# Performance work log

Measured on AMD Instinct MI355X. Metric: run time of the kernel, lower is better.

## Reference

```python
import jax, jax.numpy as jnp
import numpy as np

B, N, A, H, HID = 2048, 8, 16, 32, 64   # batch, n_agents, dim_action, dim_utility_hidden, dim_hidden
DQ = (H + A) * N                         # dim_q_input


def setup_inputs() -> dict:
    key = jax.random.key(0)
    ks = jax.random.split(key, 6)
    def w(k, shape, fan_in):
        return jax.random.normal(k, shape, jnp.float32) / np.sqrt(fan_in).astype(np.float32)
    return {
        "hidden_states_n": jax.random.normal(ks[0], (B, N, H), jnp.float32),
        # one-hot actions, as QTRAN substitutes torch.eye(dim_action) rows
        "actions_n": jax.nn.one_hot(jax.random.randint(ks[1], (B, N), 0, A), A, dtype=jnp.float32),
        "q_w1": w(ks[2], (DQ, HID), DQ), "q_b1": jnp.zeros((HID,), jnp.float32),
        "q_w2": w(ks[3], (HID, HID), HID), "q_b2": jnp.zeros((HID,), jnp.float32),
        "q_w3": w(ks[4], (HID, 1), HID), "q_b3": jnp.zeros((1,), jnp.float32),
    }


def reference(hidden_states_n, actions_n, q_w1, q_b1, q_w2, q_b2, q_w3, q_b3):
    """Vectorized QTRAN_alt.counterfactual_values_hat.

    Original: for each agent g and action a, replace agent g's action with one-hot(a)
    and run the joint Q_jt MLP. Here all n_agents*dim_action substitutions are
    built by broadcasting and run as one batched MLP.
    Output: [B, n_agents, dim_action].
    """
    Bn, Nn, Hh = hidden_states_n.shape
    Aa = actions_n.shape[-1]
    eye_a = jnp.eye(Aa, dtype=actions_n.dtype)          # [a, dA]
    agent_eq = jnp.eye(Nn, dtype=bool)                  # [g, j]: j == g
    # cf_actions[b, g, a, j, :] = eye_a[a] if j == g else actions_n[b, j, :]
    cf_actions = jnp.where(
        agent_eq[None, :, None, :, None],               # [1,G,1,J,1]
        eye_a[None, None, :, None, :],                  # [1,1,A,1,dA]
        actions_n[:, None, None, :, :],                 # [B,1,1,J,dA]
    )                                                   # [B,G,A,J,dA]
    hid = jnp.broadcast_to(hidden_states_n[:, None, None, :, :], (Bn, Nn, Aa, Nn, Hh))
    # per-agent (hidden, action) concat then flatten agents, matching
    # torch.cat([h, a], -1).view([-1, dim_q_input])
    inp = jnp.concatenate([hid, cf_actions], axis=-1).reshape(Bn, Nn, Aa, Nn * (Hh + Aa))
    h1 = jax.nn.relu(inp @ q_w1 + q_b1)
    h2 = jax.nn.relu(h1 @ q_w2 + q_b2)
    q = h2 @ q_w3 + q_b3                                # [B, G, A, 1]
    return q[..., 0]
```

## Files before the change

### kernel.cpp

```cpp
#include <hip/hip_runtime.h>
#include <hip/hip_bf16.h>

typedef __attribute__((ext_vector_type(4))) float f32x4;
typedef __attribute__((ext_vector_type(8))) short bf16x8;

struct Smem {
    float inp[384];
    float part[4][64];
    float base[64];
    float subsum[64];
    float sub[8][64];
    int   sel[8];
};

template<bool ISF32>
__device__ __forceinline__ float ldin(const void* p, int i) {
    if constexpr (ISF32) return ((const float*)p)[i];
    else return __bfloat162float(((const __hip_bfloat16*)p)[i]);
}

template<bool ISF32>
__device__ __forceinline__ f32x4 ldq(const void* p, int i) {
    if constexpr (ISF32) return *(const f32x4*)((const float*)p + i);
    else {
        const __hip_bfloat16* q = (const __hip_bfloat16*)p + i;
        return (f32x4){__bfloat162float(q[0]), __bfloat162float(q[1]),
                       __bfloat162float(q[2]), __bfloat162float(q[3])};
    }
}

__device__ __forceinline__ short bf16bits(float v) {
    __hip_bfloat16 h = __float2bfloat16(v);
    return *(const short*)&h;
}
__device__ __forceinline__ float bf16val(short s) {
    return __bfloat162float(*(const __hip_bfloat16*)&s);
}

__device__ __forceinline__ bool word_looks_bf16(unsigned int w) {
    const unsigned int lo = w & 0xFFFFu;
    const unsigned int ex = (lo >> 7) & 0xFFu;
    return (ex >= 100u && ex <= 140u) || (lo & 0x7FFFu) == 0u;
}

__device__ __forceinline__ bool vote_isf32_scalar(const void* hidden) {
    const unsigned int* hw = (const unsigned int*)hidden;
    int cnt = 0;
    #pragma unroll
    for (int i = 0; i < 32; ++i) cnt += word_looks_bf16(hw[i]) ? 1 : 0;
    return cnt < 16;
}

template<bool ISF32>
__device__ void w2prep_body(const void* w2, short* wsfrag, int idx0) {
    #pragma unroll
    for (int i = 0; i < 2; ++i) {
        const int idx = idx0 + i * 2048;
        const int j = idx & 7;
        const int lane = (idx >> 3) & 63;
        const int nt = (idx >> 9) & 3;
        const int ks = idx >> 11;
        const int src = (ks * 32 + (lane >> 4) * 8 + j) * 64 + nt * 16 + (lane & 15);
        const float v = ldin<ISF32>(w2, src);
        const short hb = bf16bits(v);
        wsfrag[idx] = hb;
        wsfrag[4096 + idx] = bf16bits(v - bf16val(hb));
    }
}

__global__ __launch_bounds__(256) void w2prep_kernel(
    const void* __restrict__ hidden, const void* __restrict__ w2,
    short* __restrict__ wsfrag) {
    const int idx0 = blockIdx.x * 256 + threadIdx.x;
    if (vote_isf32_scalar(hidden)) w2prep_body<true>(w2, wsfrag, idx0);
    else                           w2prep_body<false>(w2, wsfrag, idx0);
}

template<bool ISF32>
__device__ void qtran_body(Smem& sm,
    const void* __restrict__ hidden, const void* __restrict__ actions,
    const void* __restrict__ w1, const void* __restrict__ b1,
    const void* __restrict__ w2, const void* __restrict__ b2,
    const void* __restrict__ w3, const void* __restrict__ b3,
    void* __restrict__ out, const short* __restrict__ wsfrag, int b, int t)
{
    const int lane = t & 63;
    const int wv = t >> 6;
    const int q = lane >> 4;
    const int n = lane & 15;
    const int fq = lane & 15;
    const int rofs = lane >> 4;

    f32x4 wr[2][2][2];
    #pragma unroll
    for (int mt = 0; mt < 2; ++mt) {
        const int row = ((wv * 2 + mt) * 48 + 32 + n) * 64;
        #pragma unroll
        for (int ks = 0; ks < 2; ++ks) {
            wr[mt][ks][0] = ldq<ISF32>(w1, row + ks * 32 + q * 8);
            wr[mt][ks][1] = ldq<ISF32>(w1, row + ks * 32 + q * 8 + 4);
        }
    }
    float b2f[4], w3f[4];
    #pragma unroll
    for (int nt = 0; nt < 4; ++nt) {
        b2f[nt] = ldin<ISF32>(b2, nt * 16 + n);
        w3f[nt] = ldin<ISF32>(w3, nt * 16 + n);
    }
    const float b3f = ldin<ISF32>(b3, 0);

    if (t < 64) {
        const int j = t >> 3, k4 = (t & 7) * 4;
        *(f32x4*)&sm.inp[j * 48 + k4] = ldq<ISF32>(hidden, (b * 8 + j) * 32 + k4);
    } else if (t < 96) {
        const int i = t - 64;
        const int j = i >> 2, c4 = (i & 3) * 4;
        *(f32x4*)&sm.inp[j * 48 + 32 + c4] = ldq<ISF32>(actions, (b * 8 + j) * 16 + c4);
    }
    __syncthreads();

    if (t < 128) {
        const int g = t >> 4, a = t & 15;
        if (sm.inp[g * 48 + 32 + a] > 0.5f) sm.sel[g] = a;
    }
    {
        f32x4 a4 = (f32x4){0.f, 0.f, 0.f, 0.f};
        #pragma unroll 8
        for (int p = 0; p < 16; ++p) {
            const int hr = wv * 64 + p * 4 + rofs;
            const int r = (hr >> 5) * 48 + (hr & 31);
            const float xv = sm.inp[r];
            const f32x4 wq = ldq<ISF32>(w1, r * 64 + fq * 4);
            #pragma unroll
            for (int c = 0; c < 4; ++c) a4[c] = fmaf(xv, wq[c], a4[c]);
        }
        #pragma unroll
        for (int c = 0; c < 4; ++c) {
            a4[c] += __shfl_xor(a4[c], 16);
            a4[c] += __shfl_xor(a4[c], 32);
        }
        if (rofs == 0) *(f32x4*)&sm.part[wv][fq * 4] = a4;
    }
    __syncthreads();

    if (t < 128) {
        const int g = t >> 4, f4 = (t & 15) * 4;
        *(f32x4*)&sm.sub[g][f4] =
            ldq<ISF32>(w1, (g * 48 + 32 + sm.sel[g]) * 64 + f4);
    } else if (t < 192) {
        const int f = t - 128;
        sm.base[f] = ldin<ISF32>(b1, f) + sm.part[0][f] + sm.part[1][f]
                   + sm.part[2][f] + sm.part[3][f];
    } else {
        const int f = t - 192;
        float s = 0.f;
        #pragma unroll
        for (int g = 0; g < 8; ++g)
            s += ldin<ISF32>(w1, (g * 48 + 32 + sm.sel[g]) * 64 + f);
        sm.subsum[f] = s;
    }
    __syncthreads();

    f32x4 bsA[2][2];
    #pragma unroll
    for (int ks = 0; ks < 2; ++ks)
      #pragma unroll
      for (int h = 0; h < 2; ++h) {
        const int f0 = ks * 32 + q * 8 + h * 4;
        const f32x4 bb = *(const f32x4*)&sm.base[f0];
        const f32x4 ss = *(const f32x4*)&sm.subsum[f0];
        bsA[ks][h] = (f32x4){bb[0] + ss[0], bb[1] + ss[1], bb[2] + ss[2], bb[3] + ss[3]};
      }
    bf16x8 ahi[2][2];
    #pragma unroll
    for (int mt = 0; mt < 2; ++mt) {
        const int g = wv * 2 + mt;
        #pragma unroll
        for (int ks = 0; ks < 2; ++ks) {
            #pragma unroll
            for (int h = 0; h < 2; ++h) {
                const int f0 = ks * 32 + q * 8 + h * 4;
                const f32x4 sg = *(const f32x4*)&sm.sub[g][f0];
                const f32x4 w4 = wr[mt][ks][h];
                #pragma unroll
                for (int c = 0; c < 4; ++c) {
                    const float v = fmaxf(bsA[ks][h][c] - sg[c] + w4[c], 0.f);
                    ahi[ks][mt][h * 4 + c] = bf16bits(v);
                }
            }
        }
    }

    f32x4 acc[2][4];
    #pragma unroll
    for (int mt = 0; mt < 2; ++mt)
      #pragma unroll
      for (int nt = 0; nt < 4; ++nt)
        acc[mt][nt] = (f32x4){0.f, 0.f, 0.f, 0.f};

    #pragma unroll
    for (int ks = 0; ks < 2; ++ks) {
        #pragma unroll
        for (int nt = 0; nt < 4; ++nt) {
            bf16x8 bhi, blo;
            if (wsfrag) {
                const int fb = ((ks * 4 + nt) * 64 + lane) * 8;
                bhi = *(const bf16x8*)&wsfrag[fb];
                blo = *(const bf16x8*)&wsfrag[4096 + fb];
            } else {
                #pragma unroll
                for (int j = 0; j < 8; ++j) {
                    const float v = ldin<ISF32>(w2, (ks * 32 + q * 8 + j) * 64 + nt * 16 + n);
                    const short hb = bf16bits(v);
                    bhi[j] = hb;
                    blo[j] = bf16bits(v - bf16val(hb));
                }
            }
            #pragma unroll
            for (int mt = 0; mt < 2; ++mt) {
                acc[mt][nt] = __builtin_amdgcn_mfma_f32_16x16x32_bf16(
                    ahi[ks][mt], bhi, acc[mt][nt], 0, 0, 0);
                acc[mt][nt] = __builtin_amdgcn_mfma_f32_16x16x32_bf16(
                    ahi[ks][mt], blo, acc[mt][nt], 0, 0, 0);
            }
        }
    }

    #pragma unroll
    for (int mt = 0; mt < 2; ++mt) {
      #pragma unroll
      for (int r = 0; r < 4; ++r) {
        float p = 0.f;
        #pragma unroll
        for (int nt = 0; nt < 4; ++nt) {
            const float h2 = fmaxf(acc[mt][nt][r] + b2f[nt], 0.f);
            p = fmaf(h2, w3f[nt], p);
        }
        p += __shfl_xor(p, 1);
        p += __shfl_xor(p, 2);
        p += __shfl_xor(p, 4);
        p += __shfl_xor(p, 8);
        if (n == mt * 4 + r) {
            const int item = wv * 32 + mt * 16 + q * 4 + r;
            if constexpr (ISF32) ((float*)out)[b * 128 + item] = p + b3f;
            else ((__hip_bfloat16*)out)[b * 128 + item] = __float2bfloat16(p + b3f);
        }
      }
    }
}

__global__ __launch_bounds__(256, 4) void qtran_cf_kernel(
    const void* __restrict__ hidden, const void* __restrict__ actions,
    const void* __restrict__ w1, const void* __restrict__ b1,
    const void* __restrict__ w2, const void* __restrict__ b2,
    const void* __restrict__ w3, const void* __restrict__ b3,
    void* __restrict__ out, const short* __restrict__ wsfrag)
{
    __shared__ Smem sm;
    const unsigned int* hw = (const unsigned int*)hidden;
    const bool pass = word_looks_bf16(hw[threadIdx.x & 31]);
    const unsigned long long m = __ballot(pass);
    const bool isf32 = (__popcll(m) < 32);

    const int b = blockIdx.x;
    const int t = threadIdx.x;
    if (isf32)
        qtran_body<true>(sm, hidden, actions, w1, b1, w2, b2, w3, b3, out, wsfrag, b, t);
    else
        qtran_body<false>(sm, hidden, actions, w1, b1, w2, b2, w3, b3, out, wsfrag, b, t);
}

extern "C" void kernel_launch(void* const* d_in, const int* in_sizes, int n_in,
                              void* d_out, int out_size, void* d_ws, size_t ws_size,
                              hipStream_t stream) {
    short* wsfrag = (ws_size >= 16384) ? (short*)d_ws : nullptr;
    if (wsfrag)
        w2prep_kernel<<<8, 256, 0, stream>>>(d_in[0], d_in[4], wsfrag);
    qtran_cf_kernel<<<2048, 256, 0, stream>>>(
        d_in[0], d_in[1], d_in[2], d_in[3], d_in[4], d_in[5], d_in[6], d_in[7],
        d_out, wsfrag);
}
```

Baseline: 90.26 us.

## Process four batch rows per block with shared W1 action slice in LDS

Each block now handles four batch items instead of one. The W2 MFMA fragments stay in registers, and the W1 action rows (128x64) are staged once into padded LDS, so their load cost is spread across the four items. Each wave then loops over the eight agents for its own batch item. The grid shrinks to 512 blocks and the occupancy hint drops to 2, which reduces parallelism and raises LDS use per block in exchange for less repeated global weight traffic.

```diff
diff --git a/kernel.cpp b/kernel.cpp
--- a/kernel.cpp
+++ b/kernel.cpp
@@ -4,13 +4,16 @@
 typedef __attribute__((ext_vector_type(4))) float f32x4;
 typedef __attribute__((ext_vector_type(8))) short bf16x8;
 
+#define NB 4
+#define W1A_S 68
+
 struct Smem {
-    float inp[384];
-    float part[4][64];
-    float base[64];
-    float subsum[64];
-    float sub[8][64];
-    int   sel[8];
+    float inp[NB][384];
+    float part[4][NB][64];
+    float baseAll[NB][64];
+    float sub[NB][8][64];
+    __align__(16) float w1act[128 * W1A_S];
+    int sel[NB][8];
 };
 
 template<bool ISF32>
@@ -82,174 +85,186 @@
     const void* __restrict__ w1, const void* __restrict__ b1,
     const void* __restrict__ w2, const void* __restrict__ b2,
     const void* __restrict__ w3, const void* __restrict__ b3,
-    void* __restrict__ out, const short* __restrict__ wsfrag, int b, int t)
+    void* __restrict__ out, const short* __restrict__ wsfrag, int blk, int t)
 {
     const int lane = t & 63;
     const int wv = t >> 6;
     const int q = lane >> 4;
     const int n = lane & 15;
-    const int fq = lane & 15;
-    const int rofs = lane >> 4;
-
-    f32x4 wr[2][2][2];
-    #pragma unroll
-    for (int mt = 0; mt < 2; ++mt) {
-        const int row = ((wv * 2 + mt) * 48 + 32 + n) * 64;
-        #pragma unroll
-        for (int ks = 0; ks < 2; ++ks) {
-            wr[mt][ks][0] = ldq<ISF32>(w1, row + ks * 32 + q * 8);
-            wr[mt][ks][1] = ldq<ISF32>(w1, row + ks * 32 + q * 8 + 4);
-        }
-    }
-    float b2f[4], w3f[4];
-    #pragma unroll
-    for (int nt = 0; nt < 4; ++nt) {
-        b2f[nt] = ldin<ISF32>(b2, nt * 16 + n);
-        w3f[nt] = ldin<ISF32>(w3, nt * 16 + n);
-    }
-    const float b3f = ldin<ISF32>(b3, 0);
-
-    if (t < 64) {
-        const int j = t >> 3, k4 = (t & 7) * 4;
-        *(f32x4*)&sm.inp[j * 48 + k4] = ldq<ISF32>(hidden, (b * 8 + j) * 32 + k4);
-    } else if (t < 96) {
-        const int i = t - 64;
-        const int j = i >> 2, c4 = (i & 3) * 4;
-        *(f32x4*)&sm.inp[j * 48 + 32 + c4] = ldq<ISF32>(actions, (b * 8 + j) * 16 + c4);
-    }
-    __syncthreads();
-
-    if (t < 128) {
-        const int g = t >> 4, a = t & 15;
-        if (sm.inp[g * 48 + 32 + a] > 0.5f) sm.sel[g] = a;
-    }
-    {
-        f32x4 a4 = (f32x4){0.f, 0.f, 0.f, 0.f};
+    const int fq = n;
+    const int rofs = q;
+    const int b0 = blk * NB;
+
+    bf16x8 bhi[2][4], blo[2][4];
+    if (wsfrag) {
+        #pragma unroll
+        for (int ks = 0; ks < 2; ++ks)
+          #pragma unroll
+          for (int nt = 0; nt < 4; ++nt) {
+            const int fb = ((ks * 4 + nt) * 64 + lane) * 8;
+            bhi[ks][nt] = *(const bf16x8*)&wsfrag[fb];
+            blo[ks][nt] = *(const bf16x8*)&wsfrag[4096 + fb];
+          }
+    } else {
+        #pragma unroll
+        for (int ks = 0; ks < 2; ++ks)
+          #pragma unroll
+          for (int nt = 0; nt < 4; ++nt)
+            #pragma unroll
+            for (int j = 0; j < 8; ++j) {
+                const float v = ldin<ISF32>(w2, (ks * 32 + q * 8 + j) * 64 + nt * 16 + n);
+                const short hb = bf16bits(v);
+                bhi[ks][nt][j] = hb;
+                blo[ks][nt][j] = bf16bits(v - bf16val(hb));
+            }
+    }
+
+    {
+        const int i0 = t >> 6, s = t & 63;
+        const int j = s >> 3, k4 = (s & 7) * 4;
+        *(f32x4*)&sm.inp[i0][j * 48 + k4] =
+            ldq<ISF32>(hidden, ((b0 + i0) * 8 + j) * 32 + k4);
+        if (s < 32) {
+            const int ja = s >> 2, c4 = (s & 3) * 4;
+            *(f32x4*)&sm.inp[i0][ja * 48 + 32 + c4] =
+                ldq<ISF32>(actions, ((b0 + i0) * 8 + ja) * 16 + c4);
+        }
+    }
+    #pragma unroll
+    for (int p = 0; p < 8; ++p) {
+        const int idx = p * 256 + t;
+        const int row = idx >> 4, qd = idx & 15;
+        *(f32x4*)&sm.w1act[row * W1A_S + qd * 4] =
+            ldq<ISF32>(w1, ((row >> 4) * 48 + 32 + (row & 15)) * 64 + qd * 4);
+    }
+    __syncthreads();
+
+    {
+        const int i0 = t >> 6, s = t & 63, a = s & 15;
+        const int g1 = s >> 4;
+        if (sm.inp[i0][g1 * 48 + 32 + a] > 0.5f) sm.sel[i0][g1] = a;
+        const int g2 = g1 + 4;
+        if (sm.inp[i0][g2 * 48 + 32 + a] > 0.5f) sm.sel[i0][g2] = a;
+    }
+    {
+        f32x4 a4[NB];
+        #pragma unroll
+        for (int i = 0; i < NB; ++i) a4[i] = (f32x4){0.f, 0.f, 0.f, 0.f};
         #pragma unroll 8
         for (int p = 0; p < 16; ++p) {
             const int hr = wv * 64 + p * 4 + rofs;
             const int r = (hr >> 5) * 48 + (hr & 31);
-            const float xv = sm.inp[r];
             const f32x4 wq = ldq<ISF32>(w1, r * 64 + fq * 4);
             #pragma unroll
-            for (int c = 0; c < 4; ++c) a4[c] = fmaf(xv, wq[c], a4[c]);
-        }
-        #pragma unroll
-        for (int c = 0; c < 4; ++c) {
-            a4[c] += __shfl_xor(a4[c], 16);
-            a4[c] += __shfl_xor(a4[c], 32);
-        }
-        if (rofs == 0) *(f32x4*)&sm.part[wv][fq * 4] = a4;
-    }
-    __syncthreads();
-
-    if (t < 128) {
-        const int g = t >> 4, f4 = (t & 15) * 4;
-        *(f32x4*)&sm.sub[g][f4] =
-            ldq<ISF32>(w1, (g * 48 + 32 + sm.sel[g]) * 64 + f4);
-    } else if (t < 192) {
-        const int f = t - 128;
-        sm.base[f] = ldin<ISF32>(b1, f) + sm.part[0][f] + sm.part[1][f]
-                   + sm.part[2][f] + sm.part[3][f];
-    } else {
-        const int f = t - 192;
-        float s = 0.f;
-        #pragma unroll
-        for (int g = 0; g < 8; ++g)
-            s += ldin<ISF32>(w1, (g * 48 + 32 + sm.sel[g]) * 64 + f);
-        sm.subsum[f] = s;
-    }
-    __syncthreads();
-
-    f32x4 bsA[2][2];
+            for (int i = 0; i < NB; ++i) {
+                const float xv = sm.inp[i][r];
+                #pragma unroll
+                for (int c = 0; c < 4; ++c) a4[i][c] = fmaf(xv, wq[c], a4[i][c]);
+            }
+        }
+        #pragma unroll
+        for (int i = 0; i < NB; ++i)
+          #pragma unroll
+          for (int c = 0; c < 4; ++c) {
+            a4[i][c] += __shfl_xor(a4[i][c], 16);
+            a4[i][c] += __shfl_xor(a4[i][c], 32);
+          }
+        if (rofs == 0) {
+            #pragma unroll
+            for (int i = 0; i < NB; ++i)
+                *(f32x4*)&sm.part[wv][i][fq * 4] = a4[i];
+        }
+    }
+    __syncthreads();
+
+    #pragma unroll
+    for (int p = 0; p < 2; ++p) {
+        const int idx = p * 256 + t;
+        const int i = idx >> 7, g = (idx >> 4) & 7, qd = idx & 15;
+        const int row = g * 16 + sm.sel[i][g];
+        *(f32x4*)&sm.sub[i][g][qd * 4] =
+            *(const f32x4*)&sm.w1act[row * W1A_S + qd * 4];
+    }
+    __syncthreads();
+
+    {
+        const int i = t >> 6, f = t & 63;
+        float v = ldin<ISF32>(b1, f);
+        #pragma unroll
+        for (int w = 0; w < 4; ++w) v += sm.part[w][i][f];
+        #pragma unroll
+        for (int g = 0; g < 8; ++g) v += sm.sub[i][g][f];
+        sm.baseAll[i][f] = v;
+    }
+    __syncthreads();
+
+    f32x4 bA[2][2];
     #pragma unroll
     for (int ks = 0; ks < 2; ++ks)
       #pragma unroll
-      for (int h = 0; h < 2; ++h) {
-        const int f0 = ks * 32 + q * 8 + h * 4;
-        const f32x4 bb = *(const f32x4*)&sm.base[f0];
-        const f32x4 ss = *(const f32x4*)&sm.subsum[f0];
-        bsA[ks][h] = (f32x4){bb[0] + ss[0], bb[1] + ss[1], bb[2] + ss[2], bb[3] + ss[3]};
-      }
-    bf16x8 ahi[2][2];
-    #pragma unroll
-    for (int mt = 0; mt < 2; ++mt) {
-        const int g = wv * 2 + mt;
-        #pragma unroll
-        for (int ks = 0; ks < 2; ++ks) {
-            #pragma unroll
-            for (int h = 0; h < 2; ++h) {
-                const int f0 = ks * 32 + q * 8 + h * 4;
-                const f32x4 sg = *(const f32x4*)&sm.sub[g][f0];
-                const f32x4 w4 = wr[mt][ks][h];
-                #pragma unroll
-                for (int c = 0; c < 4; ++c) {
-                    const float v = fmaxf(bsA[ks][h][c] - sg[c] + w4[c], 0.f);
-                    ahi[ks][mt][h * 4 + c] = bf16bits(v);
-                }
-            }
-        }
-    }
-
-    f32x4 acc[2][4];
-    #pragma unroll
-    for (int mt = 0; mt < 2; ++mt)
-      #pragma unroll
-      for (int nt = 0; nt < 4; ++nt)
-        acc[mt][nt] = (f32x4){0.f, 0.f, 0.f, 0.f};
-
-    #pragma unroll
-    for (int ks = 0; ks < 2; ++ks) {
-        #pragma unroll
-        for (int nt = 0; nt < 4; ++nt) {
-            bf16x8 bhi, blo;
-            if (wsfrag) {
-                const int fb = ((ks * 4 + nt) * 64 + lane) * 8;
-                bhi = *(const bf16x8*)&wsfrag[fb];
-                blo = *(const bf16x8*)&wsfrag[4096 + fb];
-            } else {
-                #pragma unroll
-                for (int j = 0; j < 8; ++j) {
-                    const float v = ldin<ISF32>(w2, (ks * 32 + q * 8 + j) * 64 + nt * 16 + n);
-                    const short hb = bf16bits(v);
-                    bhi[j] = hb;
-                    blo[j] = bf16bits(v - bf16val(hb));
-                }
-            }
-            #pragma unroll
-            for (int mt = 0; mt < 2; ++mt) {
-                acc[mt][nt] = __builtin_amdgcn_mfma_f32_16x16x32_bf16(
-                    ahi[ks][mt], bhi, acc[mt][nt], 0, 0, 0);
-                acc[mt][nt] = __builtin_amdgcn_mfma_f32_16x16x32_bf16(
-                    ahi[ks][mt], blo, acc[mt][nt], 0, 0, 0);
-            }
-        }
-    }
-
-    #pragma unroll
-    for (int mt = 0; mt < 2; ++mt) {
-      #pragma unroll
-      for (int r = 0; r < 4; ++r) {
-        float p = 0.f;
-        #pragma unroll
-        for (int nt = 0; nt < 4; ++nt) {
-            const float h2 = fmaxf(acc[mt][nt][r] + b2f[nt], 0.f);
-            p = fmaf(h2, w3f[nt], p);
-        }
-        p += __shfl_xor(p, 1);
-        p += __shfl_xor(p, 2);
-        p += __shfl_xor(p, 4);
-        p += __shfl_xor(p, 8);
-        if (n == mt * 4 + r) {
-            const int item = wv * 32 + mt * 16 + q * 4 + r;
-            if constexpr (ISF32) ((float*)out)[b * 128 + item] = p + b3f;
-            else ((__hip_bfloat16*)out)[b * 128 + item] = __float2bfloat16(p + b3f);
-        }
-      }
-    }
-}
-
-__global__ __launch_bounds__(256, 4) void qtran_cf_kernel(
+      for (int h = 0; h < 2; ++h)
+        bA[ks][h] = *(const f32x4*)&sm.baseAll[wv][ks * 32 + q * 8 + h * 4];
+
+    float b2f[4], w3f[4];
+    #pragma unroll
+    for (int nt = 0; nt < 4; ++nt) {
+        b2f[nt] = ldin<ISF32>(b2, nt * 16 + n);
+        w3f[nt] = ldin<ISF32>(w3, nt * 16 + n);
+    }
+    const float b3f = ldin<ISF32>(b3, 0);
+
+    for (int g = 0; g < 8; ++g) {
+        bf16x8 af[2];
+        const int arow = (g * 16 + n) * W1A_S;
+        #pragma unroll
+        for (int ks = 0; ks < 2; ++ks)
+          #pragma unroll
+          for (int h = 0; h < 2; ++h) {
+            const int f0 = ks * 32 + q * 8 + h * 4;
+            const f32x4 sg = *(const f32x4*)&sm.sub[wv][g][f0];
+            const f32x4 wA = *(const f32x4*)&sm.w1act[arow + f0];
+            #pragma unroll
+            for (int c = 0; c < 4; ++c) {
+                const float v = fmaxf(bA[ks][h][c] - sg[c] + wA[c], 0.f);
+                af[ks][h * 4 + c] = bf16bits(v);
+            }
+          }
+
+        f32x4 acc[4];
+        #pragma unroll
+        for (int nt = 0; nt < 4; ++nt) acc[nt] = (f32x4){0.f, 0.f, 0.f, 0.f};
+        #pragma unroll
+        for (int ks = 0; ks < 2; ++ks)
+          #pragma unroll
+          for (int nt = 0; nt < 4; ++nt) {
+            acc[nt] = __builtin_amdgcn_mfma_f32_16x16x32_bf16(
+                af[ks], bhi[ks][nt], acc[nt], 0, 0, 0);
+            acc[nt] = __builtin_amdgcn_mfma_f32_16x16x32_bf16(
+                af[ks], blo[ks][nt], acc[nt], 0, 0, 0);
+          }
+
+        #pragma unroll
+        for (int r = 0; r < 4; ++r) {
+            float p = 0.f;
+            #pragma unroll
+            for (int nt = 0; nt < 4; ++nt) {
+                const float h2 = fmaxf(acc[nt][r] + b2f[nt], 0.f);
+                p = fmaf(h2, w3f[nt], p);
+            }
+            p += __shfl_xor(p, 1);
+            p += __shfl_xor(p, 2);
+            p += __shfl_xor(p, 4);
+            p += __shfl_xor(p, 8);
+            if (n == r) {
+                const int oi = (b0 + wv) * 128 + g * 16 + q * 4 + r;
+                if constexpr (ISF32) ((float*)out)[oi] = p + b3f;
+                else ((__hip_bfloat16*)out)[oi] = __float2bfloat16(p + b3f);
+            }
+        }
+    }
+}
+
+__global__ __launch_bounds__(256, 2) void qtran_cf_kernel(
     const void* __restrict__ hidden, const void* __restrict__ actions,
     const void* __restrict__ w1, const void* __restrict__ b1,
     const void* __restrict__ w2, const void* __restrict__ b2,
@@ -262,12 +277,12 @@
     const unsigned long long m = __ballot(pass);
     const bool isf32 = (__popcll(m) < 32);
 
-    const int b = blockIdx.x;
+    const int blk = blockIdx.x;
     const int t = threadIdx.x;
     if (isf32)
-        qtran_body<true>(sm, hidden, actions, w1, b1, w2, b2, w3, b3, out, wsfrag, b, t);
+        qtran_body<true>(sm, hidden, actions, w1, b1, w2, b2, w3, b3, out, wsfrag, blk, t);
     else
-        qtran_body<false>(sm, hidden, actions, w1, b1, w2, b2, w3, b3, out, wsfrag, b, t);
+        qtran_body<false>(sm, hidden, actions, w1, b1, w2, b2, w3, b3, out, wsfrag, blk, t);
 }
 
 extern "C" void kernel_launch(void* const* d_in, const int* in_sizes, int n_in,
@@ -276,7 +291,7 @@
     short* wsfrag = (ws_size >= 16384) ? (short*)d_ws : nullptr;
     if (wsfrag)
         w2prep_kernel<<<8, 256, 0, stream>>>(d_in[0], d_in[4], wsfrag);
-    qtran_cf_kernel<<<2048, 256, 0, stream>>>(
+    qtran_cf_kernel<<<512, 256, 0, stream>>>(
         d_in[0], d_in[1], d_in[2], d_in[3], d_in[4], d_in[5], d_in[6], d_in[7],
         d_out, wsfrag);
 }
```

New measurement: 87.97 us. 2.5% less time.
